# Kernel tuning notes

Measured on AMD Instinct MI355X. Metric: run time of the kernel, lower is better.

## Reference

```python
import jax, jax.numpy as jnp
import numpy as np

B, S, D = 4, 2048, 2048   # batch, seq, embed
E, R = 64, 64             # experts, expert_rank
INIT_SCALE = 0.02


def setup_inputs() -> dict:
    key = jax.random.key(0)
    k_x, k_m, k_up, k_dn = jax.random.split(key, 4)
    x = jax.random.normal(k_x, (B, S, D), dtype=jnp.float32)
    expert_mask = jax.random.uniform(k_m, (B, S, E), dtype=jnp.float32)
    # up_proj weight, out_first=True: [experts, rank, embed]
    w_up = jax.random.normal(k_up, (E, R, D), dtype=jnp.float32) * INIT_SCALE
    # down_proj weight, out_first=True: [embed, experts, rank]
    w_down = jax.random.normal(k_dn, (D, E, R), dtype=jnp.float32) * INIT_SCALE
    return {"x": x, "expert_mask": expert_mask, "w_up": w_up, "w_down": w_down}


def reference(x, expert_mask, w_up, w_down):
    # up projection: [B,S,D] x [E,R,D] -> [B,S,E,R]
    h = jnp.einsum("bsd,erd->bser", x, w_up)
    h = jax.nn.silu(h)
    # mask inactive experts (broadcast over rank)
    h = h * expert_mask[:, :, :, None]
    # down projection: [B,S,E,R] x [D,E,R] -> [B,S,D]
    out = jnp.einsum("bser,der->bsd", h, w_down)
    return out
```

## Files before the change

### kernel.cpp

```cpp
#include <hip/hip_runtime.h>
#include <hip/hip_bf16.h>

typedef unsigned short u16;
typedef unsigned int   u32;
typedef __attribute__((ext_vector_type(8))) short  s16x8;
typedef __attribute__((ext_vector_type(4))) float  f32x4;
typedef __attribute__((ext_vector_type(4))) unsigned short u16x4;

#define MT    8192
#define DE    2048
#define NEXP  64
#define ERDIM 4096

__device__ __forceinline__ u16 to_bf16(float f) {
  u32 u = __builtin_bit_cast(u32, f);
  u32 r = u + 0x7fffu + ((u >> 16) & 1u);
  return (u16)(r >> 16);
}

__global__ void cvt_f32_bf16(const float* __restrict__ in, u16* __restrict__ out, int n) {
  const int stride = gridDim.x * blockDim.x;
  for (int i = blockIdx.x * blockDim.x + threadIdx.x; i * 4 < n; i += stride) {
    const float4 v = *reinterpret_cast<const float4*>(in + (size_t)i * 4);
    u16x4 o;
    o.x = to_bf16(v.x); o.y = to_bf16(v.y); o.z = to_bf16(v.z); o.w = to_bf16(v.w);
    *reinterpret_cast<u16x4*>(out + (size_t)i * 4) = o;
  }
}

#define GLDS(gp, lp) __builtin_amdgcn_global_load_lds(                        \
    (const __attribute__((address_space(1))) void*)(gp),                      \
    (__attribute__((address_space(3))) void*)(lp), 16, 0, 0)

#define BAR() do { asm volatile("" ::: "memory");                             \
                   __builtin_amdgcn_s_barrier();                              \
                   asm volatile("" ::: "memory"); } while (0)

template<int FUSE, int K>
__global__ __launch_bounds__(512, 2) void gemm_bt(
    const u16* __restrict__ A, const u16* __restrict__ Bm,
    const float* __restrict__ mask, void* __restrict__ Cout,
    const int M, const int N)
{
  constexpr int BM = 256, BN = 256, BK = 32;
  constexpr int NT = K / BK;
  __shared__ __align__(16) u16 lds[65536];

  const int nbn = N / BN;
  const int nwg = (int)gridDim.x;
  const int cpx = nwg >> 3;
  const int bid = (int)blockIdx.x;
  const int swz = (bid & 7) * cpx + (bid >> 3);
  const int bm = (swz / nbn) * BM;
  const int bn = (swz % nbn) * BN;

  const int tid  = (int)threadIdx.x;
  const int lane = tid & 63;
  const int w    = tid >> 6;
  const int wr   = w >> 2;
  const int wc   = w & 3;

  const int fr = lane & 15;
  const int cp = (lane >> 4) ^ ((lane >> 1) & 3);

  const int lr = lane >> 2;
  const int cl = (lane & 3) ^ ((lane >> 3) & 3);
  const int c0 = 2 * w, c1 = 2 * w + 1;
  const u16* aS0 = A  + (size_t)(bm + c0 * 16 + lr) * K + cl * 8;
  const u16* aS1 = A  + (size_t)(bm + c1 * 16 + lr) * K + cl * 8;
  const u16* bS0 = Bm + (size_t)(bn + c0 * 16 + lr) * K + cl * 8;
  const u16* bS1 = Bm + (size_t)(bn + c1 * 16 + lr) * K + cl * 8;

  f32x4 acc[8][4] = {};

#pragma unroll
  for (int t = 0; t < 3; ++t) {
    u16* dst = lds + t * 16384;
    GLDS(aS0 + t * BK, dst +        c0 * 512);
    GLDS(aS1 + t * BK, dst +        c1 * 512);
    GLDS(bS0 + t * BK, dst + 8192 + c0 * 512);
    GLDS(bS1 + t * BK, dst + 8192 + c1 * 512);
  }
  asm volatile("s_waitcnt vmcnt(8)" ::: "memory");
  BAR();

#pragma unroll 4
  for (int t = 0; t < NT; ++t) {
    const int slot = t & 3;
    const u16* sA = lds + slot * 16384;
    const u16* sB = lds + slot * 16384 + 8192;
    u16* dst = lds + ((t + 3) & 3) * 16384;
    const bool st = (t + 3 < NT);
    const size_t koff = (size_t)(t + 3) * BK;

    s16x8 afr[4], bfr[4];
#pragma unroll
    for (int m = 0; m < 4; ++m)
      afr[m] = *reinterpret_cast<const s16x8*>(
          &sA[(wr * 128 + m * 16 + fr) * 32 + cp * 8]);
#pragma unroll
    for (int n = 0; n < 4; ++n)
      bfr[n] = *reinterpret_cast<const s16x8*>(
          &sB[(wc * 64 + n * 16 + fr) * 32 + cp * 8]);
    if (st) {
      GLDS(aS0 + koff, dst +        c0 * 512);
      GLDS(aS1 + koff, dst +        c1 * 512);
    }
    __builtin_amdgcn_s_setprio(1);
#pragma unroll
    for (int m = 0; m < 4; ++m)
#pragma unroll
      for (int n = 0; n < 4; ++n)
        acc[m][n] = __builtin_amdgcn_mfma_f32_16x16x32_bf16(
            afr[m], bfr[n], acc[m][n], 0, 0, 0);
    __builtin_amdgcn_s_setprio(0);

    s16x8 afr2[4];
#pragma unroll
    for (int m = 0; m < 4; ++m)
      afr2[m] = *reinterpret_cast<const s16x8*>(
          &sA[(wr * 128 + (4 + m) * 16 + fr) * 32 + cp * 8]);
    if (st) {
      GLDS(bS0 + koff, dst + 8192 + c0 * 512);
      GLDS(bS1 + koff, dst + 8192 + c1 * 512);
    }
    __builtin_amdgcn_s_setprio(1);
#pragma unroll
    for (int m = 0; m < 4; ++m)
#pragma unroll
      for (int n = 0; n < 4; ++n)
        acc[4 + m][n] = __builtin_amdgcn_mfma_f32_16x16x32_bf16(
            afr2[m], bfr[n], acc[4 + m][n], 0, 0, 0);
    __builtin_amdgcn_s_setprio(0);

    if (t + 3 < NT) {
      asm volatile("s_waitcnt vmcnt(8)" ::: "memory");
    } else if (t + 2 < NT) {
      asm volatile("s_waitcnt vmcnt(4)" ::: "memory");
    } else if (t + 1 < NT) {
      asm volatile("s_waitcnt vmcnt(0)" ::: "memory");
    }
    if (t + 1 < NT) BAR();
  }

  const int rgrp = (lane >> 4) * 4;
  if (FUSE) {
    u16* H = (u16*)Cout;
    const int ew = (bn + wc * 64) >> 6;
#pragma unroll
    for (int m = 0; m < 8; ++m) {
#pragma unroll
      for (int j = 0; j < 4; ++j) {
        const int grow = bm + wr * 128 + m * 16 + rgrp + j;
        const float mv = mask[(size_t)grow * NEXP + ew];
#pragma unroll
        for (int n = 0; n < 4; ++n) {
          const int gcol = bn + wc * 64 + n * 16 + fr;
          float v = acc[m][n][j];
          v = v / (1.0f + __expf(-v));
          H[(size_t)grow * N + gcol] = to_bf16(v * mv);
        }
      }
    }
  } else {
    float* O = (float*)Cout;
#pragma unroll
    for (int m = 0; m < 8; ++m) {
#pragma unroll
      for (int j = 0; j < 4; ++j) {
        const int grow = bm + wr * 128 + m * 16 + rgrp + j;
#pragma unroll
        for (int n = 0; n < 4; ++n) {
          const int gcol = bn + wc * 64 + n * 16 + fr;
          O[(size_t)grow * N + gcol] = acc[m][n][j];
        }
      }
    }
  }
}

extern "C" void kernel_launch(void* const* d_in, const int* in_sizes, int n_in,
                              void* d_out, int out_size, void* d_ws, size_t ws_size,
                              hipStream_t stream) {
  const float* x     = (const float*)d_in[0];
  const float* emask = (const float*)d_in[1];
  const float* w_up  = (const float*)d_in[2];
  const float* w_dn  = (const float*)d_in[3];
  float* out = (float*)d_out;

  const size_t need = ((size_t)MT * DE + (size_t)ERDIM * DE + (size_t)DE * ERDIM +
                       (size_t)MT * ERDIM) * sizeof(u16);
  if (ws_size < need) return;

  u16* xb  = (u16*)d_ws;
  u16* wub = xb  + (size_t)MT * DE;
  u16* wdb = wub + (size_t)ERDIM * DE;
  u16* hb  = wdb + (size_t)DE * ERDIM;

  hipLaunchKernelGGL(cvt_f32_bf16, dim3(2048), dim3(256), 0, stream, x,    xb,  MT * DE);
  hipLaunchKernelGGL(cvt_f32_bf16, dim3(1024), dim3(256), 0, stream, w_up, wub, ERDIM * DE);
  hipLaunchKernelGGL(cvt_f32_bf16, dim3(1024), dim3(256), 0, stream, w_dn, wdb, DE * ERDIM);

  hipLaunchKernelGGL((gemm_bt<1, DE>), dim3((MT / 256) * (ERDIM / 256)), dim3(512), 0, stream,
                     xb, wub, emask, (void*)hb, MT, ERDIM);
  hipLaunchKernelGGL((gemm_bt<0, ERDIM>), dim3((MT / 256) * (DE / 256)), dim3(512), 0, stream,
                     hb, wdb, nullptr, (void*)out, MT, DE);
}
```

Before: 281.8 us.

## Switch GEMM inner loop to 32x32x16 MFMA with single-barrier schedule

Replaces the 16x16x32 bf16 MFMA tiling (8x4 accumulators per wave) with 32x32x16 MFMA (4x2 f32x16 accumulators), reading each 32-wide K slab as two 16-wide halves from LDS. Each iteration now loads all fragments first, issues the prefetch, waits and barriers, then runs all MFMAs. The aim is fewer LDS fragment reads and fewer MFMA issues per tile, with the larger instruction's higher throughput. The barrier now sits before the MFMAs rather than after them, which could expose more sync latency. The epilogue is remapped to the 32x32 output layout.

```diff
diff --git a/kernel.cpp b/kernel.cpp
--- a/kernel.cpp
+++ b/kernel.cpp
@@ -3,9 +3,9 @@
 
 typedef unsigned short u16;
 typedef unsigned int   u32;
-typedef __attribute__((ext_vector_type(8))) short  s16x8;
-typedef __attribute__((ext_vector_type(4))) float  f32x4;
-typedef __attribute__((ext_vector_type(4))) unsigned short u16x4;
+typedef __attribute__((ext_vector_type(8)))  short s16x8;
+typedef __attribute__((ext_vector_type(16))) float f32x16;
+typedef __attribute__((ext_vector_type(4)))  unsigned short u16x4;
 
 #define MT    8192
 #define DE    2048
@@ -60,8 +60,14 @@
   const int wr   = w >> 2;
   const int wc   = w & 3;
 
-  const int fr = lane & 15;
-  const int cp = (lane >> 4) ^ ((lane >> 1) & 3);
+  const int l31 = lane & 31;
+  const int p0 = (lane >> 5) ^ ((lane >> 1) & 3);
+  const int p1 = p0 ^ 2;
+
+  const int aO0 = (wr * 128 + l31) * 32 + p0 * 8;
+  const int aO1 = (wr * 128 + l31) * 32 + p1 * 8;
+  const int bO0 = 8192 + (wc * 64 + l31) * 32 + p0 * 8;
+  const int bO1 = 8192 + (wc * 64 + l31) * 32 + p1 * 8;
 
   const int lr = lane >> 2;
   const int cl = (lane & 3) ^ ((lane >> 3) & 3);
@@ -71,7 +77,7 @@
   const u16* bS0 = Bm + (size_t)(bn + c0 * 16 + lr) * K + cl * 8;
   const u16* bS1 = Bm + (size_t)(bn + c1 * 16 + lr) * K + cl * 8;
 
-  f32x4 acc[8][4] = {};
+  f32x16 acc[4][2] = {};
 
 #pragma unroll
   for (int t = 0; t < 3; ++t) {
@@ -86,93 +92,87 @@
 
 #pragma unroll 4
   for (int t = 0; t < NT; ++t) {
-    const int slot = t & 3;
-    const u16* sA = lds + slot * 16384;
-    const u16* sB = lds + slot * 16384 + 8192;
-    u16* dst = lds + ((t + 3) & 3) * 16384;
-    const bool st = (t + 3 < NT);
-    const size_t koff = (size_t)(t + 3) * BK;
-
-    s16x8 afr[4], bfr[4];
-#pragma unroll
-    for (int m = 0; m < 4; ++m)
-      afr[m] = *reinterpret_cast<const s16x8*>(
-          &sA[(wr * 128 + m * 16 + fr) * 32 + cp * 8]);
-#pragma unroll
-    for (int n = 0; n < 4; ++n)
-      bfr[n] = *reinterpret_cast<const s16x8*>(
-          &sB[(wc * 64 + n * 16 + fr) * 32 + cp * 8]);
-    if (st) {
+    const u16* sl = lds + (t & 3) * 16384;
+
+    s16x8 a0[4], a1[4], b0[2], b1[2];
+#pragma unroll
+    for (int m = 0; m < 4; ++m) {
+      a0[m] = *reinterpret_cast<const s16x8*>(&sl[aO0 + m * 1024]);
+      a1[m] = *reinterpret_cast<const s16x8*>(&sl[aO1 + m * 1024]);
+    }
+#pragma unroll
+    for (int n = 0; n < 2; ++n) {
+      b0[n] = *reinterpret_cast<const s16x8*>(&sl[bO0 + n * 1024]);
+      b1[n] = *reinterpret_cast<const s16x8*>(&sl[bO1 + n * 1024]);
+    }
+
+    if (t + 3 < NT) {
+      u16* dst = lds + ((t + 3) & 3) * 16384;
+      const size_t koff = (size_t)(t + 3) * BK;
       GLDS(aS0 + koff, dst +        c0 * 512);
       GLDS(aS1 + koff, dst +        c1 * 512);
-    }
-    __builtin_amdgcn_s_setprio(1);
-#pragma unroll
-    for (int m = 0; m < 4; ++m)
-#pragma unroll
-      for (int n = 0; n < 4; ++n)
-        acc[m][n] = __builtin_amdgcn_mfma_f32_16x16x32_bf16(
-            afr[m], bfr[n], acc[m][n], 0, 0, 0);
-    __builtin_amdgcn_s_setprio(0);
-
-    s16x8 afr2[4];
-#pragma unroll
-    for (int m = 0; m < 4; ++m)
-      afr2[m] = *reinterpret_cast<const s16x8*>(
-          &sA[(wr * 128 + (4 + m) * 16 + fr) * 32 + cp * 8]);
-    if (st) {
       GLDS(bS0 + koff, dst + 8192 + c0 * 512);
       GLDS(bS1 + koff, dst + 8192 + c1 * 512);
     }
+
+    if (t + 3 < NT)      asm volatile("s_waitcnt vmcnt(8)" ::: "memory");
+    else if (t + 2 < NT) asm volatile("s_waitcnt vmcnt(4)" ::: "memory");
+    else if (t + 1 < NT) asm volatile("s_waitcnt vmcnt(0)" ::: "memory");
+
+    BAR();
+
     __builtin_amdgcn_s_setprio(1);
 #pragma unroll
     for (int m = 0; m < 4; ++m)
 #pragma unroll
-      for (int n = 0; n < 4; ++n)
-        acc[4 + m][n] = __builtin_amdgcn_mfma_f32_16x16x32_bf16(
-            afr2[m], bfr[n], acc[4 + m][n], 0, 0, 0);
+      for (int n = 0; n < 2; ++n)
+        acc[m][n] = __builtin_amdgcn_mfma_f32_32x32x16_bf16(
+            a0[m], b0[n], acc[m][n], 0, 0, 0);
+#pragma unroll
+    for (int m = 0; m < 4; ++m)
+#pragma unroll
+      for (int n = 0; n < 2; ++n)
+        acc[m][n] = __builtin_amdgcn_mfma_f32_32x32x16_bf16(
+            a1[m], b1[n], acc[m][n], 0, 0, 0);
     __builtin_amdgcn_s_setprio(0);
-
-    if (t + 3 < NT) {
-      asm volatile("s_waitcnt vmcnt(8)" ::: "memory");
-    } else if (t + 2 < NT) {
-      asm volatile("s_waitcnt vmcnt(4)" ::: "memory");
-    } else if (t + 1 < NT) {
-      asm volatile("s_waitcnt vmcnt(0)" ::: "memory");
-    }
-    if (t + 1 < NT) BAR();
-  }
-
-  const int rgrp = (lane >> 4) * 4;
+  }
+
+  const int rbase = 4 * (lane >> 5);
   if (FUSE) {
     u16* H = (u16*)Cout;
     const int ew = (bn + wc * 64) >> 6;
 #pragma unroll
-    for (int m = 0; m < 8; ++m) {
-#pragma unroll
-      for (int j = 0; j < 4; ++j) {
-        const int grow = bm + wr * 128 + m * 16 + rgrp + j;
-        const float mv = mask[(size_t)grow * NEXP + ew];
-#pragma unroll
-        for (int n = 0; n < 4; ++n) {
-          const int gcol = bn + wc * 64 + n * 16 + fr;
-          float v = acc[m][n][j];
-          v = v / (1.0f + __expf(-v));
-          H[(size_t)grow * N + gcol] = to_bf16(v * mv);
+    for (int m = 0; m < 4; ++m) {
+#pragma unroll
+      for (int q = 0; q < 4; ++q) {
+#pragma unroll
+        for (int j = 0; j < 4; ++j) {
+          const int grow = bm + wr * 128 + m * 32 + j + 8 * q + rbase;
+          const float mv = mask[(size_t)grow * NEXP + ew];
+#pragma unroll
+          for (int n = 0; n < 2; ++n) {
+            const int gcol = bn + wc * 64 + n * 32 + l31;
+            float v = acc[m][n][q * 4 + j];
+            v = v / (1.0f + __expf(-v));
+            H[(size_t)grow * N + gcol] = to_bf16(v * mv);
+          }
         }
       }
     }
   } else {
     float* O = (float*)Cout;
 #pragma unroll
-    for (int m = 0; m < 8; ++m) {
-#pragma unroll
-      for (int j = 0; j < 4; ++j) {
-        const int grow = bm + wr * 128 + m * 16 + rgrp + j;
-#pragma unroll
-        for (int n = 0; n < 4; ++n) {
-          const int gcol = bn + wc * 64 + n * 16 + fr;
-          O[(size_t)grow * N + gcol] = acc[m][n][j];
+    for (int m = 0; m < 4; ++m) {
+#pragma unroll
+      for (int q = 0; q < 4; ++q) {
+#pragma unroll
+        for (int j = 0; j < 4; ++j) {
+          const int grow = bm + wr * 128 + m * 32 + j + 8 * q + rbase;
+#pragma unroll
+          for (int n = 0; n < 2; ++n) {
+            const int gcol = bn + wc * 64 + n * 32 + l31;
+            O[(size_t)grow * N + gcol] = acc[m][n][q * 4 + j];
+          }
         }
       }
     }
```

After: 308.7 us. +9.6%, slower.
